# Optimization experiments

Hardware: AMD Instinct MI355X
Metric: run time of the kernel (lower is better)

## Reference

```python
import jax, jax.numpy as jnp
import numpy as np

NEG_MIN = float(np.finfo(np.float32).min)
LN_EPS = 1e-05


def _layer_norm(x, g, b):
    m = jnp.mean(x, axis=-1, keepdims=True)
    v = jnp.var(x, axis=-1, keepdims=True)
    return (x - m) * jax.lax.rsqrt(v + LN_EPS) * g + b


def _rel_shift_uni(x):
    # x: [qlen, rlen, bsz, n_head] -- Transformer-XL relative shift
    q, r, b, n = x.shape
    zero_pad = jnp.zeros((q, 1, b, n), x.dtype)
    x_padded = jnp.concatenate([zero_pad, x], axis=1).reshape(r + 1, q, b, n)
    return x_padded[1:].reshape(q, r, b, n)


def setup_inputs() -> dict:
    key = jax.random.key(0)
    ks = jax.random.split(key, 12)
    qlen, bsz, d_model = 2048, 2, 1024
    n_head, d_head, d_inner = 16, 64, 4096

    w = jax.random.normal(ks[0], (qlen, bsz, d_model), dtype=jnp.float32)

    # sinusoidal relative position embedding, positions klen-1 .. 0
    pos_seq = jnp.arange(qlen - 1, -1, -1, dtype=jnp.float32)
    inv_freq = 1.0 / (10000.0 ** (jnp.arange(0, d_model, 2, dtype=jnp.float32) / d_model))
    sinusoid = pos_seq[:, None] * inv_freq[None, :]
    r = jnp.concatenate([jnp.sin(sinusoid), jnp.cos(sinusoid)], axis=-1)  # [qlen, d_model]

    s = 0.02
    r_w_bias = jax.random.normal(ks[1], (n_head, d_head), dtype=jnp.float32) * s
    r_r_bias = jax.random.normal(ks[2], (n_head, d_head), dtype=jnp.float32) * s
    qkv_w = jax.random.normal(ks[3], (d_model, 3 * n_head * d_head), dtype=jnp.float32) * s
    r_net_w = jax.random.normal(ks[4], (d_model, n_head * d_head), dtype=jnp.float32) * s
    o_w = jax.random.normal(ks[5], (n_head * d_head, d_model), dtype=jnp.float32) * s
    ffn_w1 = jax.random.normal(ks[6], (d_model, d_inner), dtype=jnp.float32) * s
    ffn_b1 = jnp.zeros((d_inner,), dtype=jnp.float32)
    ffn_w2 = jax.random.normal(ks[7], (d_inner, d_model), dtype=jnp.float32) * s
    ffn_b2 = jnp.zeros((d_model,), dtype=jnp.float32)
    ln1_g = jnp.ones((d_model,), dtype=jnp.float32)
    ln1_b = jnp.zeros((d_model,), dtype=jnp.float32)
    ln2_g = jnp.ones((d_model,), dtype=jnp.float32)
    ln2_b = jnp.zeros((d_model,), dtype=jnp.float32)

    # causal mask: position j > i is masked (uni-directional attention)
    attn_mask = jnp.triu(jnp.ones((qlen, qlen), dtype=bool), k=1)

    return {"w": w, "r": r, "r_w_bias": r_w_bias, "r_r_bias": r_r_bias,
            "attn_mask": attn_mask, "qkv_w": qkv_w, "r_net_w": r_net_w, "o_w": o_w,
            "ln1_g": ln1_g, "ln1_b": ln1_b, "ffn_w1": ffn_w1, "ffn_b1": ffn_b1,
            "ffn_w2": ffn_w2, "ffn_b2": ffn_b2, "ln2_g": ln2_g, "ln2_b": ln2_b}


def reference(w, r, r_w_bias, r_r_bias, attn_mask, qkv_w, r_net_w, o_w,
              ln1_g, ln1_b, ffn_w1, ffn_b1, ffn_w2, ffn_b2, ln2_g, ln2_b):
    qlen, bsz, d_model = w.shape
    n_head, d_head = r_w_bias.shape
    scale = 1.0 / (d_head ** 0.5)

    # qkv projection (post-lnorm path: no pre-norm)
    w_heads = w @ qkv_w  # [q, b, 3*n*d]
    w_q, w_k, w_v = jnp.split(w_heads, 3, axis=-1)
    w_q = w_q.reshape(qlen, bsz, n_head, d_head)
    w_k = w_k.reshape(qlen, bsz, n_head, d_head)
    w_v = w_v.reshape(qlen, bsz, n_head, d_head)

    r_k = (r @ r_net_w).reshape(r.shape[0], n_head, d_head)  # [rlen, n, d]

    # AC: content term, BD: position term with rel-shift
    AC = jnp.einsum('ibnd,jbnd->ijbn', w_q + r_w_bias, w_k)
    BD = jnp.einsum('ibnd,jnd->ijbn', w_q + r_r_bias, r_k)
    BD = _rel_shift_uni(BD)

    attn_score = (AC + BD) * scale
    attn_score = jnp.where(attn_mask[:, :, None, None], NEG_MIN, attn_score)
    attn_prob = jax.nn.softmax(attn_score, axis=1)  # softmax over key axis j

    attn_vec = jnp.einsum('ijbn,jbnd->ibnd', attn_prob, w_v)
    attn_vec = attn_vec.reshape(qlen, bsz, n_head * d_head)
    attn_out = attn_vec @ o_w

    x = _layer_norm(w + attn_out, ln1_g, ln1_b)  # post-lnorm

    # PositionwiseFF (post-lnorm, eval: dropout inactive)
    core = jax.nn.relu(x @ ffn_w1 + ffn_b1) @ ffn_w2 + ffn_b2
    out = _layer_norm(x + core, ln2_g, ln2_b)
    return out
```

## Files before the change

kernel.cpp:

```cpp
#include <hip/hip_runtime.h>
#include <math.h>


typedef __attribute__((ext_vector_type(8))) short short8;
typedef __attribute__((ext_vector_type(4))) float floatx4;

__device__ inline unsigned short f2bf(float f) {
  union { float f; unsigned u; } v; v.f = f;
  unsigned r = v.u + 0x7FFFu + ((v.u >> 16) & 1u);
  return (unsigned short)(r >> 16);
}
__device__ inline float bf2f(unsigned short u) {
  union { unsigned u; float f; } v; v.u = ((unsigned)u) << 16; return v.f;
}

__global__ __launch_bounds__(256) void prep_kernel(
    const float* __restrict__ w, unsigned short* __restrict__ wb,
    const float* __restrict__ r, unsigned short* __restrict__ rb,
    const float* __restrict__ qkv_w, unsigned short* __restrict__ qkvT,
    const float* __restrict__ r_net_w, unsigned short* __restrict__ rnetT,
    const float* __restrict__ o_w, unsigned short* __restrict__ owT,
    const float* __restrict__ ffn_w1, unsigned short* __restrict__ w1T,
    const float* __restrict__ ffn_w2, unsigned short* __restrict__ w2T) {
  __shared__ __align__(16) unsigned short Ts[64][68];
  const int blk = blockIdx.x;
  const int t = threadIdx.x;
  if (blk < 6144) {
    const float* in = blk < 4096 ? w : r;
    unsigned short* outp = blk < 4096 ? wb : rb;
    const int i = (blk < 4096 ? blk : blk - 4096) * 256 + t;
    float4 v = ((const float4*)in)[i];
    ((ushort4*)outp)[i] =
        make_ushort4(f2bf(v.x), f2bf(v.y), f2bf(v.z), f2bf(v.w));
    return;
  }
  const float* src; unsigned short* dst; int K, N, idx;
  if (blk < 6912)      { src = qkv_w;   dst = qkvT;  K = 1024; N = 3072; idx = blk - 6144; }
  else if (blk < 7168) { src = r_net_w; dst = rnetT; K = 1024; N = 1024; idx = blk - 6912; }
  else if (blk < 7424) { src = o_w;     dst = owT;   K = 1024; N = 1024; idx = blk - 7168; }
  else if (blk < 8448) { src = ffn_w1;  dst = w1T;   K = 1024; N = 4096; idx = blk - 7424; }
  else                 { src = ffn_w2;  dst = w2T;   K = 4096; N = 1024; idx = blk - 8448; }
  const int nbx = N >> 6;
  const int k0 = (idx / nbx) * 64, n0 = (idx % nbx) * 64;
  const int rr = t >> 4, c = (t & 15) * 4;
#pragma unroll
  for (int rb2 = 0; rb2 < 64; rb2 += 16) {
    float4 v = *(const float4*)(src + (size_t)(k0 + rb2 + rr) * N + n0 + c);
    *(ushort4*)&Ts[rb2 + rr][c] =
        make_ushort4(f2bf(v.x), f2bf(v.y), f2bf(v.z), f2bf(v.w));
  }
  __syncthreads();
#pragma unroll
  for (int rb2 = 0; rb2 < 64; rb2 += 16) {
    const int nn = rb2 + rr;
    ushort4 o = make_ushort4(Ts[c + 0][nn], Ts[c + 1][nn],
                             Ts[c + 2][nn], Ts[c + 3][nn]);
    *(ushort4*)(dst + (size_t)(n0 + nn) * K + k0 + c) = o;
  }
}

template<int BIAS, int RELU, int OUT_BF16>
__global__ __launch_bounds__(256) void bgemm_kernel(
    const unsigned short* __restrict__ A, const unsigned short* __restrict__ Bt,
    const float* __restrict__ bias, void* __restrict__ C,
    int M, int N, int Kstride, int Klen, size_t psize) {
  __shared__ __align__(16) unsigned short As[128 * 32];
  __shared__ __align__(16) unsigned short Bs[128 * 32];
  const int t = threadIdx.x;
  const int wv = t >> 6, lane = t & 63, quad = lane >> 4, lq = lane & 15;
  const int m0 = blockIdx.y * 128, n0 = blockIdx.x * 128;
  const int kz = blockIdx.z;
  const int wvm = (wv >> 1) * 64, wvn = (wv & 1) * 64;

  const int srow = t >> 2;
  const int scol = (t & 3) * 8;
  const size_t koff = (size_t)kz * Klen;
  const unsigned short* Ag = A + (size_t)(m0 + srow) * Kstride + scol + koff;
  const unsigned short* Bg = Bt + (size_t)(n0 + srow) * Kstride + scol + koff;
  unsigned short* AsW = As + (size_t)wv * 512;
  unsigned short* BsW = Bs + (size_t)wv * 512;

  floatx4 acc[4][4];
#pragma unroll
  for (int am = 0; am < 4; ++am)
#pragma unroll
    for (int bn = 0; bn < 4; ++bn) acc[am][bn] = (floatx4){0.f, 0.f, 0.f, 0.f};

  for (int k0 = 0; k0 < Klen; k0 += 32) {
    __syncthreads();
    __builtin_amdgcn_global_load_lds(
        (const __attribute__((address_space(1))) void*)(Ag + k0),
        (__attribute__((address_space(3))) void*)AsW, 16, 0, 0);
    __builtin_amdgcn_global_load_lds(
        (const __attribute__((address_space(1))) void*)(Ag + (size_t)64 * Kstride + k0),
        (__attribute__((address_space(3))) void*)(AsW + 64 * 32), 16, 0, 0);
    __builtin_amdgcn_global_load_lds(
        (const __attribute__((address_space(1))) void*)(Bg + k0),
        (__attribute__((address_space(3))) void*)BsW, 16, 0, 0);
    __builtin_amdgcn_global_load_lds(
        (const __attribute__((address_space(1))) void*)(Bg + (size_t)64 * Kstride + k0),
        (__attribute__((address_space(3))) void*)(BsW + 64 * 32), 16, 0, 0);
    __syncthreads();

    short8 af[4], bf[4];
#pragma unroll
    for (int am = 0; am < 4; ++am)
      af[am] = *(const short8*)&As[(wvm + am * 16 + lq) * 32 + quad * 8];
#pragma unroll
    for (int bn = 0; bn < 4; ++bn)
      bf[bn] = *(const short8*)&Bs[(wvn + bn * 16 + lq) * 32 + quad * 8];
#pragma unroll
    for (int am = 0; am < 4; ++am)
#pragma unroll
      for (int bn = 0; bn < 4; ++bn)
        acc[am][bn] = __builtin_amdgcn_mfma_f32_16x16x32_bf16(
            af[am], bf[bn], acc[am][bn], 0, 0, 0);
  }

  float bs[4] = {0.f, 0.f, 0.f, 0.f};
  if (BIAS) {
    if (kz == 0) {
#pragma unroll
      for (int bn = 0; bn < 4; ++bn) bs[bn] = bias[n0 + wvn + bn * 16 + lq];
    }
  }
  float* Cf = (float*)C + (size_t)kz * psize;
#pragma unroll
  for (int am = 0; am < 4; ++am) {
#pragma unroll
    for (int u = 0; u < 4; ++u) {
      const size_t row = m0 + wvm + am * 16 + quad * 4 + u;
#pragma unroll
      for (int bn = 0; bn < 4; ++bn) {
        const size_t col = n0 + wvn + bn * 16 + lq;
        float v = acc[am][bn][u];
        if (BIAS) v += bs[bn];
        if (RELU) v = fmaxf(v, 0.f);
        if (OUT_BF16) ((unsigned short*)C)[row * N + col] = f2bf(v);
        else          Cf[row * N + col] = v;
      }
    }
  }
}

__global__ __launch_bounds__(512, 4) void attn_mfma_kernel(
    const unsigned short* __restrict__ w_heads,
    const unsigned short* __restrict__ r_k,
    const float* __restrict__ r_w_bias, const float* __restrict__ r_r_bias,
    unsigned short* __restrict__ attn_vec) {
  __shared__ __align__(16) unsigned short Ks[64 * 72];
  __shared__ __align__(16) unsigned short Vt[64 * 72];
  __shared__ __align__(16) unsigned short Rb[256 * 72];
  __shared__ __align__(16) unsigned short Pl[8 * 16 * 72];

  const int t = threadIdx.x;
  const int wv = t >> 6, lane = t & 63, quad = lane >> 4, lq = lane & 15;
  const int g = blockIdx.x;
  const int qq = g >> 5, bnb = g & 31;
  const int it = (qq < 8) ? (15 - qq) : (qq - 8);
  const int b = bnb & 1, n = bnb >> 1;
  const int i0 = it * 128, iw = i0 + wv * 16;

  const int kr = t >> 3, kc8 = (t & 7) * 8;
  const int vj = t >> 4, vc = (t & 15) * 4;

  short8 qw[2], qr[2];
  {
    const unsigned short* qrow =
        w_heads + (size_t)((iw + lq) * 2 + b) * 3072 + n * 64;
    short8 a0 = *(const short8*)(qrow + quad * 8);
    short8 a1 = *(const short8*)(qrow + 32 + quad * 8);
    const float* wbp = r_w_bias + n * 64;
    const float* rbp = r_r_bias + n * 64;
#pragma unroll
    for (int j = 0; j < 8; ++j) {
      const int k0 = quad * 8 + j, k1 = 32 + quad * 8 + j;
      const float q0 = bf2f((unsigned short)a0[j]);
      const float q1 = bf2f((unsigned short)a1[j]);
      qw[0][j] = (short)f2bf(q0 + wbp[k0]);
      qr[0][j] = (short)f2bf(q0 + rbp[k0]);
      qw[1][j] = (short)f2bf(q1 + wbp[k1]);
      qr[1][j] = (short)f2bf(q1 + rbp[k1]);
    }
  }

  floatx4 o[4];
#pragma unroll
  for (int dt = 0; dt < 4; ++dt) o[dt] = (floatx4){0.f, 0.f, 0.f, 0.f};
  float lrow[4] = {0.f, 0.f, 0.f, 0.f};

  unsigned short* Pw = Pl + wv * (16 * 72);
  const int wb2 = 112 - wv * 16;

  int g_idx[4]; bool g_hi[4];
#pragma unroll
  for (int u = 0; u < 4; ++u) {
    const int s = 15 - (quad * 4 + u);
    g_idx[u] = quad * 16 + ((s + lq) & 15);
    g_hi[u] = (s + lq) >= 16;
  }

  const int pbase0 = 1920 - i0;
  const int jt_end = 2 * it + 2;

#pragma unroll
  for (int bq = 0; bq < 2; ++bq) {
    const int row = pbase0 + bq * 64 + kr;
    const int slot = row & 255;
    *(short8*)&Rb[slot * 72 + kc8] =
        *(const short8*)(r_k + (size_t)row * 1024 + n * 64 + kc8);
  }
  short8 sK, sR;
  ushort4 sVl, sVh;
  {
    const unsigned short* kb =
        w_heads + (size_t)(kr * 2 + b) * 3072 + n * 64 + 1024 + kc8;
    sK = *(const short8*)kb;
    const unsigned short* vbp =
        w_heads + (size_t)((2 * vj) * 2 + b) * 3072 + n * 64 + 2048 + vc;
    sVl = *(const ushort4*)vbp;
    sVh = *(const ushort4*)(vbp + 2 * 3072);
    int pg = pbase0 + 128 + kr; if (pg > 2047) pg = 2047;
    sR = *(const short8*)(r_k + (size_t)pg * 1024 + n * 64 + kc8);
  }

  for (int jt = 0; jt < jt_end; ++jt) {
    const int j0 = jt * 64;
    const int pbase = pbase0 + 64 * jt;
    __syncthreads();

    *(short8*)&Ks[kr * 72 + kc8] = sK;
#pragma unroll
    for (int i2 = 0; i2 < 4; ++i2)
      *(unsigned*)&Vt[(vc + i2) * 72 + 2 * vj] =
          (unsigned)sVl[i2] | ((unsigned)sVh[i2] << 16);
    {
      const int slot = (pbase + 128 + kr) & 255;
      *(short8*)&Rb[slot * 72 + kc8] = sR;
    }

    if (jt + 1 < jt_end) {
      const int j0n = j0 + 64;
      const unsigned short* kb =
          w_heads + (size_t)((j0n + kr) * 2 + b) * 3072 + n * 64 + 1024 + kc8;
      sK = *(const short8*)kb;
      const unsigned short* vbp =
          w_heads + (size_t)((j0n + 2 * vj) * 2 + b) * 3072 + n * 64 + 2048 + vc;
      sVl = *(const ushort4*)vbp;
      sVh = *(const ushort4*)(vbp + 2 * 3072);
      int pg = pbase + 192 + kr; if (pg > 2047) pg = 2047;
      sR = *(const short8*)(r_k + (size_t)pg * 1024 + n * 64 + kc8);
    }
    __syncthreads();

    floatx4 ac[4];
#pragma unroll
    for (int ct = 0; ct < 4; ++ct) {
      short8 b0 = *(const short8*)&Ks[(ct * 16 + lq) * 72 + quad * 8];
      short8 b1 = *(const short8*)&Ks[(ct * 16 + lq) * 72 + 32 + quad * 8];
      floatx4 z = (floatx4){0.f, 0.f, 0.f, 0.f};
      z = __builtin_amdgcn_mfma_f32_16x16x32_bf16(qw[0], b0, z, 0, 0, 0);
      z = __builtin_amdgcn_mfma_f32_16x16x32_bf16(qw[1], b1, z, 0, 0, 0);
      ac[ct] = z;
    }
    floatx4 Tt[5];
#pragma unroll
    for (int pt = 0; pt < 5; ++pt) {
      const int slot = (pbase + wb2 + pt * 16 + lq) & 255;
      short8 b0 = *(const short8*)&Rb[slot * 72 + quad * 8];
      short8 b1 = *(const short8*)&Rb[slot * 72 + 32 + quad * 8];
      floatx4 z = (floatx4){0.f, 0.f, 0.f, 0.f};
      z = __builtin_amdgcn_mfma_f32_16x16x32_bf16(qr[0], b0, z, 0, 0, 0);
      z = __builtin_amdgcn_mfma_f32_16x16x32_bf16(qr[1], b1, z, 0, 0, 0);
      Tt[pt] = z;
    }

#pragma unroll
    for (int u = 0; u < 4; ++u) {
      const int r = quad * 4 + u, i = iw + r;
      float sh[5];
#pragma unroll
      for (int pt = 0; pt < 5; ++pt) sh[pt] = __shfl(Tt[pt][u], g_idx[u]);
#pragma unroll
      for (int ct = 0; ct < 4; ++ct) {
        const float bd = g_hi[u] ? sh[ct + 1] : sh[ct];
        const int j = j0 + ct * 16 + lq;
        const float pr =
            (j <= i) ? __expf((ac[ct][u] + bd) * 0.125f) : 0.f;
        Pw[r * 72 + ct * 16 + lq] = f2bf(pr);
        lrow[u] += pr;
      }
    }

    __builtin_amdgcn_s_waitcnt(0xC07F);

    short8 pA0 = *(const short8*)&Pw[lq * 72 + quad * 8];
    short8 pA1 = *(const short8*)&Pw[lq * 72 + 32 + quad * 8];
#pragma unroll
    for (int dt = 0; dt < 4; ++dt) {
      short8 v0 = *(const short8*)&Vt[(dt * 16 + lq) * 72 + quad * 8];
      short8 v1 = *(const short8*)&Vt[(dt * 16 + lq) * 72 + 32 + quad * 8];
      o[dt] = __builtin_amdgcn_mfma_f32_16x16x32_bf16(pA0, v0, o[dt], 0, 0, 0);
      o[dt] = __builtin_amdgcn_mfma_f32_16x16x32_bf16(pA1, v1, o[dt], 0, 0, 0);
    }
  }

#pragma unroll
  for (int u = 0; u < 4; ++u) {
    float l = lrow[u];
    l += __shfl_xor(l, 1);
    l += __shfl_xor(l, 2);
    l += __shfl_xor(l, 4);
    l += __shfl_xor(l, 8);
    const float linv = 1.f / l;
    const int i = iw + quad * 4 + u;
    unsigned short* op = attn_vec + (size_t)(i * 2 + b) * 1024 + n * 64 + lq;
#pragma unroll
    for (int dt = 0; dt < 4; ++dt) op[dt * 16] = f2bf(o[dt][u] * linv);
  }
}

__global__ __launch_bounds__(256) void ln_res_kernel(
    const float* __restrict__ X, const float* __restrict__ R0,
    const float* __restrict__ R1,
    const float* __restrict__ g, const float* __restrict__ bta,
    float* __restrict__ out, unsigned short* __restrict__ out_bf) {
  const int row = blockIdx.x;
  const int t = threadIdx.x;
  float4 xv = ((const float4*)(X + (size_t)row * 1024))[t];
  float4 rv = ((const float4*)(R0 + (size_t)row * 1024))[t];
  float4 v = make_float4(xv.x + rv.x, xv.y + rv.y, xv.z + rv.z, xv.w + rv.w);
  if (R1) {
    float4 r2 = ((const float4*)(R1 + (size_t)row * 1024))[t];
    v.x += r2.x; v.y += r2.y; v.z += r2.z; v.w += r2.w;
  }
  float s  = v.x + v.y + v.z + v.w;
  float sq = v.x * v.x + v.y * v.y + v.z * v.z + v.w * v.w;
#pragma unroll
  for (int off = 32; off > 0; off >>= 1) {
    s  += __shfl_xor(s, off);
    sq += __shfl_xor(sq, off);
  }
  __shared__ float ss[4], ssq[4];
  const int wid = t >> 6;
  if ((t & 63) == 0) { ss[wid] = s; ssq[wid] = sq; }
  __syncthreads();
  s  = ss[0] + ss[1] + ss[2] + ss[3];
  sq = ssq[0] + ssq[1] + ssq[2] + ssq[3];
  const float mean = s * (1.f / 1024.f);
  const float var  = sq * (1.f / 1024.f) - mean * mean;
  const float inv  = rsqrtf(var + 1e-5f);
  float4 gv = ((const float4*)g)[t];
  float4 bv = ((const float4*)bta)[t];
  float4 ov = make_float4((v.x - mean) * inv * gv.x + bv.x,
                          (v.y - mean) * inv * gv.y + bv.y,
                          (v.z - mean) * inv * gv.z + bv.z,
                          (v.w - mean) * inv * gv.w + bv.w);
  ((float4*)(out + (size_t)row * 1024))[t] = ov;
  if (out_bf)
    ((ushort4*)(out_bf + (size_t)row * 1024))[t] =
        make_ushort4(f2bf(ov.x), f2bf(ov.y), f2bf(ov.z), f2bf(ov.w));
}

extern "C" void kernel_launch(void* const* d_in, const int* in_sizes, int n_in,
                              void* d_out, int out_size, void* d_ws, size_t ws_size,
                              hipStream_t stream) {
  (void)in_sizes; (void)n_in; (void)out_size; (void)ws_size;
  const float* w        = (const float*)d_in[0];
  const float* r        = (const float*)d_in[1];
  const float* r_w_bias = (const float*)d_in[2];
  const float* r_r_bias = (const float*)d_in[3];
  const float* qkv_w    = (const float*)d_in[5];
  const float* r_net_w  = (const float*)d_in[6];
  const float* o_w      = (const float*)d_in[7];
  const float* ln1_g    = (const float*)d_in[8];
  const float* ln1_b    = (const float*)d_in[9];
  const float* ffn_w1   = (const float*)d_in[10];
  const float* ffn_b1   = (const float*)d_in[11];
  const float* ffn_w2   = (const float*)d_in[12];
  const float* ffn_b2   = (const float*)d_in[13];
  const float* ln2_g    = (const float*)d_in[14];
  const float* ln2_b    = (const float*)d_in[15];
  float* out = (float*)d_out;

  char* base = (char*)d_ws;
  const size_t MB = (size_t)1 << 20;
  unsigned short* w_heads = (unsigned short*)(base + 0);
  float*          aout0   = (float*)(base + 0);
  float*          aout1   = (float*)(base + 16 * MB);
  unsigned short* h1      = (unsigned short*)(base + 0);
  float*          x       = (float*)(base + 32 * MB);
  unsigned short* w2T     = (unsigned short*)(base + 48 * MB);
  unsigned short* w1T     = (unsigned short*)(base + 56 * MB);
  float*          core0   = (float*)(base + 56 * MB);
  float*          core1   = (float*)(base + 72 * MB);
  unsigned short* wb      = (unsigned short*)(base + 64 * MB);
  unsigned short* avec    = (unsigned short*)(base + 64 * MB);
  unsigned short* rb      = (unsigned short*)(base + 72 * MB);
  unsigned short* xb      = (unsigned short*)(base + 72 * MB);
  unsigned short* rk      = (unsigned short*)(base + 76 * MB);
  unsigned short* qkvT    = (unsigned short*)(base + 80 * MB);
  unsigned short* owT     = (unsigned short*)(base + 86 * MB);
  unsigned short* rnetT   = (unsigned short*)(base + 88 * MB);

  dim3 blk(256);
  prep_kernel<<<9472, blk, 0, stream>>>(w, wb, r, rb, qkv_w, qkvT,
                                        r_net_w, rnetT, o_w, owT,
                                        ffn_w1, w1T, ffn_w2, w2T);

  bgemm_kernel<0, 0, 1><<<dim3(24, 32, 1), blk, 0, stream>>>(
      wb, qkvT, nullptr, w_heads, 4096, 3072, 1024, 1024, 0);
  bgemm_kernel<0, 0, 1><<<dim3(8, 16, 1), blk, 0, stream>>>(
      rb, rnetT, nullptr, rk, 2048, 1024, 1024, 1024, 0);
  attn_mfma_kernel<<<512, 512, 0, stream>>>(
      w_heads, rk, r_w_bias, r_r_bias, avec);
  bgemm_kernel<0, 0, 0><<<dim3(8, 32, 2), blk, 0, stream>>>(
      avec, owT, nullptr, aout0, 4096, 1024, 1024, 512, (size_t)4096 * 1024);
  ln_res_kernel<<<4096, blk, 0, stream>>>(w, aout0, aout1, ln1_g, ln1_b, x, xb);
  bgemm_kernel<1, 1, 1><<<dim3(32, 32, 1), blk, 0, stream>>>(
      xb, w1T, ffn_b1, h1, 4096, 4096, 1024, 1024, 0);
  bgemm_kernel<1, 0, 0><<<dim3(8, 32, 2), blk, 0, stream>>>(
      h1, w2T, ffn_b2, core0, 4096, 1024, 4096, 2048, (size_t)4096 * 1024);
  ln_res_kernel<<<4096, blk, 0, stream>>>(x, core0, core1, ln2_g, ln2_b, out, nullptr);
}
```

Measured before the change: 455.0 us.

## Double GEMM k-step, merge QKV and r_k GEMMs, remap V-load threads

The GEMM main loop now stages 64 K-elements per barrier pair: two 32-wide sub-tiles are loaded into doubled LDS buffers and then consumed, which halves the number of __syncthreads per K sweep. The QKV and r_k projections are merged into one launch of 896 blocks, removing a kernel launch and letting the small r_k GEMM fill the tail of the larger one. Separately, the attention kernel's V-tile load mapping (vj/vc) is permuted, which changes the global and LDS access pattern. The cost is twice the GEMM LDS footprint, which can lower occupancy.

```diff
diff --git a/kernel.cpp b/kernel.cpp
--- a/kernel.cpp
+++ b/kernel.cpp
@@ -60,16 +60,15 @@
 }
 
 template<int BIAS, int RELU, int OUT_BF16>
-__global__ __launch_bounds__(256) void bgemm_kernel(
+__device__ __forceinline__ void bgemm_body(
     const unsigned short* __restrict__ A, const unsigned short* __restrict__ Bt,
     const float* __restrict__ bias, void* __restrict__ C,
-    int M, int N, int Kstride, int Klen, size_t psize) {
-  __shared__ __align__(16) unsigned short As[128 * 32];
-  __shared__ __align__(16) unsigned short Bs[128 * 32];
+    int M, int N, int Kstride, int Klen, size_t psize,
+    int bx, int by, int kz,
+    unsigned short* As, unsigned short* Bs) {
   const int t = threadIdx.x;
   const int wv = t >> 6, lane = t & 63, quad = lane >> 4, lq = lane & 15;
-  const int m0 = blockIdx.y * 128, n0 = blockIdx.x * 128;
-  const int kz = blockIdx.z;
+  const int m0 = by * 128, n0 = bx * 128;
   const int wvm = (wv >> 1) * 64, wvn = (wv & 1) * 64;
 
   const int srow = t >> 2;
@@ -77,8 +76,10 @@
   const size_t koff = (size_t)kz * Klen;
   const unsigned short* Ag = A + (size_t)(m0 + srow) * Kstride + scol + koff;
   const unsigned short* Bg = Bt + (size_t)(n0 + srow) * Kstride + scol + koff;
-  unsigned short* AsW = As + (size_t)wv * 512;
-  unsigned short* BsW = Bs + (size_t)wv * 512;
+  unsigned short* AsW0 = As + (size_t)wv * 512;
+  unsigned short* AsW1 = As + 4096 + (size_t)wv * 512;
+  unsigned short* BsW0 = Bs + (size_t)wv * 512;
+  unsigned short* BsW1 = Bs + 4096 + (size_t)wv * 512;
 
   floatx4 acc[4][4];
 #pragma unroll
@@ -86,35 +87,52 @@
 #pragma unroll
     for (int bn = 0; bn < 4; ++bn) acc[am][bn] = (floatx4){0.f, 0.f, 0.f, 0.f};
 
-  for (int k0 = 0; k0 < Klen; k0 += 32) {
+  for (int k0 = 0; k0 < Klen; k0 += 64) {
     __syncthreads();
     __builtin_amdgcn_global_load_lds(
         (const __attribute__((address_space(1))) void*)(Ag + k0),
-        (__attribute__((address_space(3))) void*)AsW, 16, 0, 0);
+        (__attribute__((address_space(3))) void*)AsW0, 16, 0, 0);
     __builtin_amdgcn_global_load_lds(
         (const __attribute__((address_space(1))) void*)(Ag + (size_t)64 * Kstride + k0),
-        (__attribute__((address_space(3))) void*)(AsW + 64 * 32), 16, 0, 0);
+        (__attribute__((address_space(3))) void*)(AsW0 + 64 * 32), 16, 0, 0);
+    __builtin_amdgcn_global_load_lds(
+        (const __attribute__((address_space(1))) void*)(Ag + k0 + 32),
+        (__attribute__((address_space(3))) void*)AsW1, 16, 0, 0);
+    __builtin_amdgcn_global_load_lds(
+        (const __attribute__((address_space(1))) void*)(Ag + (size_t)64 * Kstride + k0 + 32),
+        (__attribute__((address_space(3))) void*)(AsW1 + 64 * 32), 16, 0, 0);
     __builtin_amdgcn_global_load_lds(
         (const __attribute__((address_space(1))) void*)(Bg + k0),
-        (__attribute__((address_space(3))) void*)BsW, 16, 0, 0);
+        (__attribute__((address_space(3))) void*)BsW0, 16, 0, 0);
     __builtin_amdgcn_global_load_lds(
         (const __attribute__((address_space(1))) void*)(Bg + (size_t)64 * Kstride + k0),
-        (__attribute__((address_space(3))) void*)(BsW + 64 * 32), 16, 0, 0);
+        (__attribute__((address_space(3))) void*)(BsW0 + 64 * 32), 16, 0, 0);
+    __builtin_amdgcn_global_load_lds(
+        (const __attribute__((address_space(1))) void*)(Bg + k0 + 32),
+        (__attribute__((address_space(3))) void*)BsW1, 16, 0, 0);
+    __builtin_amdgcn_global_load_lds(
+        (const __attribute__((address_space(1))) void*)(Bg + (size_t)64 * Kstride + k0 + 32),
+        (__attribute__((address_space(3))) void*)(BsW1 + 64 * 32), 16, 0, 0);
     __syncthreads();
 
-    short8 af[4], bf[4];
-#pragma unroll
-    for (int am = 0; am < 4; ++am)
-      af[am] = *(const short8*)&As[(wvm + am * 16 + lq) * 32 + quad * 8];
-#pragma unroll
-    for (int bn = 0; bn < 4; ++bn)
-      bf[bn] = *(const short8*)&Bs[(wvn + bn * 16 + lq) * 32 + quad * 8];
-#pragma unroll
-    for (int am = 0; am < 4; ++am)
+#pragma unroll
+    for (int s = 0; s < 2; ++s) {
+      const unsigned short* Asub = s ? As + 4096 : As;
+      const unsigned short* Bsub = s ? Bs + 4096 : Bs;
+      short8 af[4], bf[4];
+#pragma unroll
+      for (int am = 0; am < 4; ++am)
+        af[am] = *(const short8*)&Asub[(wvm + am * 16 + lq) * 32 + quad * 8];
 #pragma unroll
       for (int bn = 0; bn < 4; ++bn)
-        acc[am][bn] = __builtin_amdgcn_mfma_f32_16x16x32_bf16(
-            af[am], bf[bn], acc[am][bn], 0, 0, 0);
+        bf[bn] = *(const short8*)&Bsub[(wvn + bn * 16 + lq) * 32 + quad * 8];
+#pragma unroll
+      for (int am = 0; am < 4; ++am)
+#pragma unroll
+        for (int bn = 0; bn < 4; ++bn)
+          acc[am][bn] = __builtin_amdgcn_mfma_f32_16x16x32_bf16(
+              af[am], bf[bn], acc[am][bn], 0, 0, 0);
+    }
   }
 
   float bs[4] = {0.f, 0.f, 0.f, 0.f};
@@ -140,6 +158,35 @@
         else          Cf[row * N + col] = v;
       }
     }
+  }
+}
+
+template<int BIAS, int RELU, int OUT_BF16>
+__global__ __launch_bounds__(256) void bgemm_kernel(
+    const unsigned short* __restrict__ A, const unsigned short* __restrict__ Bt,
+    const float* __restrict__ bias, void* __restrict__ C,
+    int M, int N, int Kstride, int Klen, size_t psize) {
+  __shared__ __align__(16) unsigned short As[2 * 128 * 32];
+  __shared__ __align__(16) unsigned short Bs[2 * 128 * 32];
+  bgemm_body<BIAS, RELU, OUT_BF16>(A, Bt, bias, C, M, N, Kstride, Klen, psize,
+                                   blockIdx.x, blockIdx.y, blockIdx.z, As, Bs);
+}
+
+__global__ __launch_bounds__(256) void qkv_rk_kernel(
+    const unsigned short* __restrict__ wb, const unsigned short* __restrict__ qkvT,
+    unsigned short* __restrict__ w_heads,
+    const unsigned short* __restrict__ rbf, const unsigned short* __restrict__ rnetT,
+    unsigned short* __restrict__ rk) {
+  __shared__ __align__(16) unsigned short As[2 * 128 * 32];
+  __shared__ __align__(16) unsigned short Bs[2 * 128 * 32];
+  const int bid = blockIdx.x;
+  if (bid < 768) {
+    bgemm_body<0, 0, 1>(wb, qkvT, nullptr, w_heads, 4096, 3072, 1024, 1024, 0,
+                        bid % 24, bid / 24, 0, As, Bs);
+  } else {
+    const int b2 = bid - 768;
+    bgemm_body<0, 0, 1>(rbf, rnetT, nullptr, rk, 2048, 1024, 1024, 1024, 0,
+                        b2 % 8, b2 / 8, 0, As, Bs);
   }
 }
 
@@ -162,7 +209,7 @@
   const int i0 = it * 128, iw = i0 + wv * 16;
 
   const int kr = t >> 3, kc8 = (t & 7) * 8;
-  const int vj = t >> 4, vc = (t & 15) * 4;
+  const int vj = t & 31, vc = (t >> 5) * 4;
 
   short8 qw[2], qr[2];
   {
@@ -408,10 +455,7 @@
                                         r_net_w, rnetT, o_w, owT,
                                         ffn_w1, w1T, ffn_w2, w2T);
 
-  bgemm_kernel<0, 0, 1><<<dim3(24, 32, 1), blk, 0, stream>>>(
-      wb, qkvT, nullptr, w_heads, 4096, 3072, 1024, 1024, 0);
-  bgemm_kernel<0, 0, 1><<<dim3(8, 16, 1), blk, 0, stream>>>(
-      rb, rnetT, nullptr, rk, 2048, 1024, 1024, 1024, 0);
+  qkv_rk_kernel<<<896, blk, 0, stream>>>(wb, qkvT, w_heads, rb, rnetT, rk);
   attn_mfma_kernel<<<512, 512, 0, stream>>>(
       w_heads, rk, r_w_bias, r_r_bias, avec);
   bgemm_kernel<0, 0, 0><<<dim3(8, 32, 2), blk, 0, stream>>>(
```

After: 428.6 us. 1.06x faster.
